# Performance work log

Hardware: AMD Instinct MI355X
Metric: run time of the kernel (lower is better)

Reference implementation:

```python
import math
import jax, jax.numpy as jnp
import numpy as np

N = 1600; C_IN = 16; HID = 64; OUT = 64; D_K = 8; N_HEADS = 8
CUTS = 8; NUM_RBF = 8; RBF_PROJ = 4; RADIUS = 6.0; ALPHA = 3.0

def leaky(x):
    return jnp.where(x >= 0, x, 0.2 * x)

def group_norm(x, gamma, beta, groups=4, eps=1e-5):
    # x: [N, C]; torch GroupNorm applied on [1, C, N]: stats over (C/groups, N) per group
    n, c = x.shape
    xg = x.T.reshape(groups, -1)
    mu = jnp.mean(xg, axis=1, keepdims=True)
    var = jnp.mean((xg - mu) ** 2, axis=1, keepdims=True)
    xn = ((xg - mu) * jax.lax.rsqrt(var + eps)).reshape(c, n).T
    return xn * gamma + beta

def setup_inputs():
    key = jax.random.key(0)
    ks = jax.random.split(key, 32)
    def rn(k, shape, s=0.1):
        return (jax.random.normal(k, shape) * s).astype(jnp.float32)
    return {
        "points": jax.random.normal(ks[0], (N, 3), jnp.float32),
        "nuv": jax.random.normal(ks[1], (N, 3, 3), jnp.float32),
        "features": jax.random.normal(ks[2], (N, C_IN), jnp.float32),
        "w_in1": rn(ks[3], (HID, C_IN)), "b_in1": rn(ks[4], (HID,)),
        "w_in2": rn(ks[5], (HID, HID)), "b_in2": rn(ks[6], (HID,)),
        "g_in": 1.0 + rn(ks[7], (HID,)), "be_in": rn(ks[8], (HID,)),
        "wq": rn(ks[9], (HID, HID)), "bq": rn(ks[10], (HID,)),
        "wk": rn(ks[11], (HID, HID)), "bk": rn(ks[12], (HID,)),
        "wv": rn(ks[13], (HID, HID)), "bv": rn(ks[14], (HID,)),
        "conv_w1": rn(ks[15], (CUTS, 4 + RBF_PROJ), 0.5),
        "conv_b1": jnp.abs(rn(ks[16], (CUTS,), 0.5)),
        "conv_w2": rn(ks[17], (HID, CUTS), 0.3), "conv_b2": rn(ks[18], (HID,), 0.3),
        "rbf_log_sigma": jnp.log(jnp.asarray(0.6 * 2.0 / (NUM_RBF - 1), jnp.float32)),
        "rbf_a": rn(ks[19], (RBF_PROJ, NUM_RBF), 0.3), "rbf_b": rn(ks[20], (RBF_PROJ,), 0.1),
        "rbf_centers": jnp.linspace(0.0, 2.0, NUM_RBF, dtype=jnp.float32),
        "w_o1": rn(ks[21], (OUT, HID)), "b_o1": rn(ks[22], (OUT,)),
        "w_o2": rn(ks[23], (OUT, OUT)), "b_o2": rn(ks[24], (OUT,)),
        "g_out": 1.0 + rn(ks[25], (OUT,)), "be_out": rn(ks[26], (OUT,)),
        "w_res": rn(ks[27], (OUT, C_IN)), "b_res": rn(ks[28], (OUT,)),
    }

def reference(points, nuv, features, w_in1, b_in1, w_in2, b_in2, g_in, be_in,
              wq, bq, wk, bk, wv, bv, conv_w1, conv_b1, conv_w2, conv_b2,
              rbf_log_sigma, rbf_a, rbf_b, rbf_centers,
              w_o1, b_o1, w_o2, b_o2, g_out, be_out, w_res, b_res):
    # point-wise MLP + GroupNorm
    h = leaky(features @ w_in1.T + b_in1)
    h = leaky(h @ w_in2.T + b_in2)
    h = group_norm(h, g_in, be_in)
    Q = h @ wq.T + bq
    K = h @ wk.T + bk
    V = h @ wv.T + bv
    pts = points / (math.sqrt(2.0) * RADIUS)
    diff = pts[None, :, :] - pts[:, None, :]            # [N, N, 3] = x_j - x_i
    n_i = nuv[:, 0, :]
    n_j = jax.lax.stop_gradient(n_i)                    # j-side normals are detached in the original
    ndot = jnp.einsum("ia,ja->ij", n_i, n_j)            # <n_i, n_j>
    d2 = jnp.sum(diff ** 2, axis=-1) * (2.0 - ndot) ** 2  # pseudo-geodesic squared distance
    W = (1.0 + d2 / ALPHA) ** (-ALPHA)                  # geodesic window weight
    d2_safe = jnp.where(d2 > 0, d2, 1.0)
    base_d = jnp.where(d2 > 0, jnp.sqrt(d2_safe), 0.0)  # safe sqrt (finite grad at 0)
    sigma = jnp.maximum(jnp.exp(rbf_log_sigma), 1e-6)
    R = jnp.exp(-((base_d[:, :, None] - rbf_centers) ** 2) / (2.0 * sigma ** 2))  # [N,N,NUM_RBF]
    R_proj = R @ rbf_a.T + rbf_b                        # [N, N, RBF_PROJ]
    X_loc = jnp.einsum("iab,ijb->ija", nuv, diff)       # local tangent-frame coords [N,N,3]
    X = jnp.concatenate([X_loc, ndot[:, :, None], R_proj], axis=-1)  # [N, N, 4+RBF_PROJ]
    F1 = jax.nn.relu(X @ conv_w1.T + conv_b1)           # shared conv layer-1 [N, N, CUTS]
    scale = 1.0 / math.sqrt(D_K)
    heads = []
    for h_id in range(N_HEADS):
        s = slice(h_id * D_K, (h_id + 1) * D_K)
        Fh = jax.nn.relu(F1 @ conv_w2[s].T + conv_b2[s])      # per-head conv weights [N, N, D_K]
        S = (Q[:, s] @ K[:, s].T) * scale                     # attention logits [N, N]
        P = jax.nn.softmax(S, axis=1) * W                     # softmax over j, fused with window
        heads.append(jnp.einsum("ij,ijc,jc->ic", P, Fh, V[:, s]))
    agg = jnp.concatenate(heads, axis=1)                      # [N, HID]
    o = leaky(agg @ w_o1.T + b_o1)
    o = leaky(o @ w_o2.T + b_o2)
    o = group_norm(o, g_out, be_out)
    return o + features @ w_res.T + b_res
```

## Files before the change

kernel.cpp:

```cpp
#include <hip/hip_runtime.h>

typedef __fp16 h2 __attribute__((ext_vector_type(2)));
typedef unsigned int u32;

#define NPTS 1600
#define NCHUNK 10
#define CHUNKJ 160
#define TILE 32
#define QS (0.35355339059327373f*1.4426950408889634f)
#define PSCALE 0.11785113019775793f
#define LOG2E 1.4426950408889634f

__device__ __forceinline__ float leaky(float x){ return x >= 0.f ? x : 0.2f*x; }
__device__ __forceinline__ float d4(float4 a, float4 b){ return a.x*b.x + a.y*b.y + a.z*b.z + a.w*b.w; }
__device__ __forceinline__ u32 pkn(float a, float b){ h2 v; v[0]=(__fp16)a; v[1]=(__fp16)b; return __builtin_bit_cast(u32,v); }
__device__ __forceinline__ h2 u2h(u32 u){ return __builtin_bit_cast(h2,u); }
__device__ __forceinline__ float dot2(h2 a, h2 b, float c){ return __builtin_amdgcn_fdot2(a,b,c,false); }
__device__ __forceinline__ u32 rfl(u32 x){ return (u32)__builtin_amdgcn_readfirstlane((int)x); }

__global__ __launch_bounds__(256) void k_in(
    const float* __restrict__ feat, const float* __restrict__ w1, const float* __restrict__ b1,
    const float* __restrict__ w2, const float* __restrict__ b2,
    const float* __restrict__ conv_w1, const float* __restrict__ conv_b1,
    const float* __restrict__ conv_w2,
    const float* __restrict__ rbf_a, const float* __restrict__ rbf_b,
    const float* __restrict__ rbf_ls, const float* __restrict__ rbf_c,
    float* __restrict__ h2out, float* __restrict__ bstat1, float* __restrict__ wpk)
{
  __shared__ float sh[4][64];
  __shared__ float sred[4][8];
  int t = threadIdx.x, w = t>>6, c = t&63;
  int i = blockIdx.x*4 + w;

  if (blockIdx.x == 0) {
    u32* wp = (u32*)wpk;
    {
      int row = t>>2, q = t&3;
      wp[32 + row*4 + q] = pkn(conv_w2[row*8+2*q], conv_w2[row*8+2*q+1]);
    }
    if (t < 32) {
      int cc = t>>2, kq = t&3;
      float a0=0.f, a1=0.f;
      #pragma unroll
      for (int p=0;p<4;p++){ a0 += conv_w1[cc*8+4+p]*rbf_a[p*8+2*kq]; a1 += conv_w1[cc*8+4+p]*rbf_a[p*8+2*kq+1]; }
      wp[cc*4+kq] = pkn(a0,a1);
    } else if (t < 40) {
      int cc = t-32; float s = conv_b1[cc];
      #pragma unroll
      for (int p=0;p<4;p++) s += conv_w1[cc*8+4+p]*rbf_b[p];
      wpk[288+cc] = s;
    } else if (t == 40) {
      float sig = fmaxf(expf(rbf_ls[0]), 1e-6f);
      float m = -LOG2E/(2.f*sig*sig);
      float c0 = rbf_c[0];
      float dl = rbf_c[1] - rbf_c[0];
      wpk[296] = c0;
      wpk[297] = m;
      wpk[298] = -2.f*m*dl;
      wpk[299] = m*dl*dl;
    }
  }

  const float4* f4 = (const float4*)(feat + i*16);
  float4 f0=f4[0], f1v=f4[1], f2v=f4[2], f3v=f4[3];
  const float4* w1r = (const float4*)(w1 + c*16);
  float h1 = b1[c] + d4(f0,w1r[0]) + d4(f1v,w1r[1]) + d4(f2v,w1r[2]) + d4(f3v,w1r[3]);
  h1 = leaky(h1);
  sh[w][c] = h1;
  __syncthreads();
  float hh = b2[c];
  #pragma unroll
  for (int k4=0;k4<16;k4++){
    float4 hv = *(const float4*)&sh[w][k4*4];
    hh += d4(hv, *(const float4*)&w2[c*64 + k4*4]);
  }
  hh = leaky(hh);
  h2out[i*64+c] = hh;

  float s = hh, qq = hh*hh;
  s += __shfl_xor(s,1);  qq += __shfl_xor(qq,1);
  s += __shfl_xor(s,2);  qq += __shfl_xor(qq,2);
  s += __shfl_xor(s,4);  qq += __shfl_xor(qq,4);
  s += __shfl_xor(s,8);  qq += __shfl_xor(qq,8);
  if ((c&15)==0){ int g=c>>4; sred[w][g]=s; sred[w][4+g]=qq; }
  __syncthreads();
  if (t<8) bstat1[blockIdx.x*8+t] = sred[0][t]+sred[1][t]+sred[2][t]+sred[3][t];
}

__global__ __launch_bounds__(256) void k_qkv(
  const float* __restrict__ h2b, const float* __restrict__ bstat1,
  const float* __restrict__ g_in, const float* __restrict__ be_in,
  const float* __restrict__ wq, const float* __restrict__ bq,
  const float* __restrict__ wk, const float* __restrict__ bk,
  const float* __restrict__ wv, const float* __restrict__ bv,
  float* __restrict__ Q, float* __restrict__ K, float* __restrict__ V)
{
  __shared__ float sh[4][64];
  __shared__ float sp[64];
  __shared__ float sst[8];
  int t=threadIdx.x, w=t>>6, c=t&63;
  int i = blockIdx.x*4 + w;
  if (t<64){ int g=t&7; float s=0.f;
    for (int m=t>>3; m<400; m+=8) s += bstat1[m*8+g];
    sp[t]=s; }
  __syncthreads();
  if (t<8){ float s=0.f;
    #pragma unroll
    for (int q=0;q<8;q++) s += sp[q*8+t];
    sst[t]=s; }
  __syncthreads();
  int g = c>>4;
  const float inv = 1.f/25600.f;
  float mu = sst[g]*inv;
  float var = sst[4+g]*inv - mu*mu;
  float rs = rsqrtf(var + 1e-5f);
  float hn = (h2b[i*64+c]-mu)*rs*g_in[c] + be_in[c];
  sh[w][c] = hn;
  __syncthreads();
  float q=bq[c], k=bk[c], v=bv[c];
  #pragma unroll
  for (int k4=0;k4<16;k4++){
    float4 hv = *(const float4*)&sh[w][k4*4];
    q += d4(hv, *(const float4*)&wq[c*64+k4*4]);
    k += d4(hv, *(const float4*)&wk[c*64+k4*4]);
    v += d4(hv, *(const float4*)&wv[c*64+k4*4]);
  }
  Q[i*64+c] = q*QS;
  K[i*64+c] = k;
  V[i*64+c] = v;
}

__global__ __launch_bounds__(256) void k_pair(
  const float* __restrict__ Qm, const float* __restrict__ Km, const float* __restrict__ Vm,
  const float* __restrict__ pts, const float* __restrict__ nuv,
  const float* __restrict__ w1, const float* __restrict__ wpk,
  const float* __restrict__ b2g, float* __restrict__ part)
{
  __shared__ __align__(16) float SM[4928];
  float* sQ  = SM;
  float* sK  = SM + 1088;
  u32*   sVp = (u32*)(SM + 3264);
  u32*   sWX = (u32*)(SM + 4352);
  float* sPt = SM + 4672;
  float* sNj = SM + 4800;
  float* sRed = SM;

  int t = threadIdx.x;
  int r = t & 15, jl = t >> 4;
  int bx = blockIdx.x;
  int rb = bx % 100, jc = bx / 100;
  int I0 = rb*16, J0 = jc*CHUNKJ;
  int i = I0 + r;

  { int row = t>>4, col = (t&15)<<2;
    *(float4*)&sQ[row*68+col] = *(const float4*)&Qm[(I0+row)*64 + col]; }
  if (t < 128) {
    int r2 = t>>3, cc = t&7, ib = (I0+r2)*9;
    float a0=w1[cc*8], a1=w1[cc*8+1], a2=w1[cc*8+2];
    float x = a0*nuv[ib+0] + a1*nuv[ib+3] + a2*nuv[ib+6];
    float y = a0*nuv[ib+1] + a1*nuv[ib+4] + a2*nuv[ib+7];
    float z = a0*nuv[ib+2] + a1*nuv[ib+5] + a2*nuv[ib+8];
    sWX[r2*20+cc*2+0] = pkn(x,y);
    sWX[r2*20+cc*2+1] = pkn(z, w1[cc*8+3]);
  }
  __syncthreads();
  u32 wxp[16];
  #pragma unroll
  for (int q2=0;q2<4;q2++) *(uint4*)&wxp[q2*4] = *(const uint4*)&sWX[r*20+q2*4];

  const u32* wp = (const u32*)wpk;
  h2 wr[8][4];
  #pragma unroll
  for (int cc=0;cc<8;cc++)
    #pragma unroll
    for (int q2=0;q2<4;q2++) wr[cc][q2] = u2h(rfl(wp[cc*4+q2]));
  const u32* w2p = wp + 32;
  const float* b1p = wpk + 288;
  float c0  = wpk[296];
  float mco = wpk[297];
  float C2  = wpk[298];
  float A1  = wpk[299];

  float pix = pts[i*3+0]*PSCALE, piy = pts[i*3+1]*PSCALE, piz = pts[i*3+2]*PSCALE;
  float nix = nuv[i*9+0], niy = nuv[i*9+1], niz = nuv[i*9+2];

  float acc[64];
  #pragma unroll
  for (int o=0;o<64;o++) acc[o] = 0.f;
  float lh[8];
  #pragma unroll
  for (int h=0;h<8;h++) lh[h] = 0.f;

  #pragma unroll 1
  for (int tb=0; tb<CHUNKJ; tb+=TILE) {
    int jbase = J0 + tb;
    __syncthreads();
    #pragma unroll
    for (int q2=0;q2<2;q2++) {
      int idx = t + q2*256;
      int row = idx >> 4, col = (idx & 15) << 2;
      *(float4*)&sK[row*68+col] = *(const float4*)&Km[(jbase+row)*64+col];
    }
    { int row = t>>4, col = (t&15)<<2;
      float4 a = *(const float4*)&Vm[(jbase+row)*64+col];
      float4 b = *(const float4*)&Vm[(jbase+16+row)*64+col];
      uint4 p; p.x=pkn(a.x,b.x); p.y=pkn(a.y,b.y); p.z=pkn(a.z,b.z); p.w=pkn(a.w,b.w);
      *(uint4*)&sVp[row*68+col] = p;
    }
    if (t < TILE) {
      int j = jbase + t;
      sPt[t*4+0]=pts[j*3+0]*PSCALE; sPt[t*4+1]=pts[j*3+1]*PSCALE; sPt[t*4+2]=pts[j*3+2]*PSCALE;
      sNj[t*4+0]=nuv[j*9+0]; sNj[t*4+1]=nuv[j*9+1]; sNj[t*4+2]=nuv[j*9+2];
    }
    __syncthreads();

    h2 F1p[2][4];
    float Wv[2];
    #pragma unroll
    for (int jj=0;jj<2;jj++) {
      int jloc = jl + (jj<<4);
      float dx = sPt[jloc*4+0]-pix, dy = sPt[jloc*4+1]-piy, dz = sPt[jloc*4+2]-piz;
      float ndot = nix*sNj[jloc*4+0] + niy*sNj[jloc*4+1] + niz*sNj[jloc*4+2];
      float d2r = dx*dx + dy*dy + dz*dz;
      float wf = 2.f - ndot;
      float d2 = d2r*wf*wf;
      float tp = fmaf(d2, 0.3333333333333333f, 1.f);
      Wv[jj] = __builtin_amdgcn_rcpf(tp*tp*tp);
      float dd = __builtin_amdgcn_sqrtf(d2);
      float g0 = dd - c0;
      float s2 = mco*g0*g0;
      float uu = C2*g0;
      float R[8];
      #pragma unroll
      for (int k=0;k<8;k++){
        float kf = (float)k, k2f = (float)(k*k);
        R[k] = __builtin_amdgcn_exp2f(fmaf(kf, uu, fmaf(k2f, A1, s2)));
      }
      h2 xv0; xv0[0]=(__fp16)dx; xv0[1]=(__fp16)dy;
      h2 xv1; xv1[0]=(__fp16)dz; xv1[1]=(__fp16)ndot;
      h2 r01=__builtin_amdgcn_cvt_pkrtz(R[0],R[1]);
      h2 r23=__builtin_amdgcn_cvt_pkrtz(R[2],R[3]);
      h2 r45=__builtin_amdgcn_cvt_pkrtz(R[4],R[5]);
      h2 r67=__builtin_amdgcn_cvt_pkrtz(R[6],R[7]);
      float F1f[8];
      #pragma unroll
      for (int cc=0;cc<8;cc++){
        float f = dot2(r67, wr[cc][3], b1p[cc]);
        f = dot2(r45, wr[cc][2], f);
        f = dot2(r23, wr[cc][1], f);
        f = dot2(r01, wr[cc][0], f);
        f = dot2(u2h(wxp[cc*2+1]), xv1, f);
        f = dot2(u2h(wxp[cc*2+0]), xv0, f);
        F1f[cc] = fmaxf(f, 0.f);
      }
      F1p[jj][0]=__builtin_amdgcn_cvt_pkrtz(F1f[0],F1f[1]);
      F1p[jj][1]=__builtin_amdgcn_cvt_pkrtz(F1f[2],F1f[3]);
      F1p[jj][2]=__builtin_amdgcn_cvt_pkrtz(F1f[4],F1f[5]);
      F1p[jj][3]=__builtin_amdgcn_cvt_pkrtz(F1f[6],F1f[7]);
    }

    #pragma unroll
    for (int h=0;h<8;h++) {
      float4 q0 = *(const float4*)&sQ[r*68+h*8];
      float4 q1 = *(const float4*)&sQ[r*68+h*8+4];
      float4 ka0 = *(const float4*)&sK[jl*68+h*8];
      float4 ka1 = *(const float4*)&sK[jl*68+h*8+4];
      float4 kb0 = *(const float4*)&sK[(jl+16)*68+h*8];
      float4 kb1 = *(const float4*)&sK[(jl+16)*68+h*8+4];
      float S0 = d4(q0,ka0) + d4(q1,ka1);
      float S1 = d4(q0,kb0) + d4(q1,kb1);
      float e0 = __builtin_amdgcn_exp2f(S0);
      float e1 = __builtin_amdgcn_exp2f(S1);
      lh[h] += e0 + e1;
      h2 ewp; ewp[0]=(__fp16)(e0*Wv[0]); ewp[1]=(__fp16)(e1*Wv[1]);
      uint4 vpA = *(const uint4*)&sVp[jl*68+h*8];
      uint4 vpB = *(const uint4*)&sVp[jl*68+h*8+4];
      u32 vparr[8] = {vpA.x,vpA.y,vpA.z,vpA.w,vpB.x,vpB.y,vpB.z,vpB.w};
      #pragma unroll
      for (int cc=0;cc<8;cc++){
        int rw = h*8+cc;
        h2 w0=u2h(w2p[rw*4+0]), w1h=u2h(w2p[rw*4+1]), w2h=u2h(w2p[rw*4+2]), w3h=u2h(w2p[rw*4+3]);
        float b2v = b2g[rw];
        float fh0 = dot2(F1p[0][0],w0, dot2(F1p[0][1],w1h, dot2(F1p[0][2],w2h, dot2(F1p[0][3],w3h, b2v))));
        float fh1 = dot2(F1p[1][0],w0, dot2(F1p[1][1],w1h, dot2(F1p[1][2],w2h, dot2(F1p[1][3],w3h, b2v))));
        h2 fhp = __builtin_amdgcn_cvt_pkrtz(fmaxf(fh0,0.f), fmaxf(fh1,0.f));
        h2 ev = u2h(vparr[cc]) * ewp;
        acc[rw] = dot2(fhp, ev, acc[rw]);
      }
    }
  }

  #pragma unroll
  for (int o=0;o<64;o++){ acc[o] += __shfl_xor(acc[o],16); acc[o] += __shfl_xor(acc[o],32); }
  #pragma unroll
  for (int h=0;h<8;h++){ lh[h] += __shfl_xor(lh[h],16); lh[h] += __shfl_xor(lh[h],32); }
  __syncthreads();
  int wv = t >> 6, lane = t & 63;
  if (lane < 16) {
    #pragma unroll
    for (int o=0;o<64;o++) sRed[(wv*16+lane)*72+o] = acc[o];
    #pragma unroll
    for (int h=0;h<8;h++) sRed[(wv*16+lane)*72+64+h] = lh[h];
  }
  __syncthreads();
  for (int v2 = t; v2 < 16*72; v2 += 256) {
    int rr = v2/72, o = v2 - rr*72;
    part[(jc*NPTS + I0 + rr)*72 + o] =
      sRed[(0*16+rr)*72+o] + sRed[(1*16+rr)*72+o] + sRed[(2*16+rr)*72+o] + sRed[(3*16+rr)*72+o];
  }
}

__global__ __launch_bounds__(256) void k_agg(
  const float* __restrict__ part, const float* __restrict__ w_o1, const float* __restrict__ b_o1,
  const float* __restrict__ w_o2, const float* __restrict__ b_o2,
  float* __restrict__ o2b, float* __restrict__ bstat2)
{
  __shared__ float sh[4][64];
  __shared__ float sred[4][8];
  int t = threadIdx.x, w = t>>6, c = t&63;
  int i = blockIdx.x*4 + w;
  int h = c>>3;
  float a = 0.f, L = 0.f;
  #pragma unroll
  for (int jc=0;jc<NCHUNK;jc++){
    const float* p = part + (jc*NPTS + i)*72;
    a += p[c]; L += p[64+h];
  }
  float agg = a / L;
  sh[w][c] = agg; __syncthreads();
  float o1 = b_o1[c];
  #pragma unroll
  for (int k4=0;k4<16;k4++){
    float4 hv = *(const float4*)&sh[w][k4*4];
    o1 += d4(hv, *(const float4*)&w_o1[c*64+k4*4]);
  }
  o1 = leaky(o1);
  __syncthreads();
  sh[w][c] = o1; __syncthreads();
  float o2 = b_o2[c];
  #pragma unroll
  for (int k4=0;k4<16;k4++){
    float4 hv = *(const float4*)&sh[w][k4*4];
    o2 += d4(hv, *(const float4*)&w_o2[c*64+k4*4]);
  }
  o2 = leaky(o2);
  o2b[i*64+c] = o2;

  float s = o2, qq = o2*o2;
  s += __shfl_xor(s,1);  qq += __shfl_xor(qq,1);
  s += __shfl_xor(s,2);  qq += __shfl_xor(qq,2);
  s += __shfl_xor(s,4);  qq += __shfl_xor(qq,4);
  s += __shfl_xor(s,8);  qq += __shfl_xor(qq,8);
  if ((c&15)==0){ int g=c>>4; sred[w][g]=s; sred[w][4+g]=qq; }
  __syncthreads();
  if (t<8) bstat2[blockIdx.x*8+t] = sred[0][t]+sred[1][t]+sred[2][t]+sred[3][t];
}

__global__ __launch_bounds__(256) void k_out(
  const float* __restrict__ o2b, const float* __restrict__ bstat2,
  const float* __restrict__ g_out, const float* __restrict__ be_out,
  const float* __restrict__ feat, const float* __restrict__ w_res, const float* __restrict__ b_res,
  float* __restrict__ out)
{
  __shared__ float sp[64];
  __shared__ float sst[8];
  int t = threadIdx.x, w = t>>6, c = t&63;
  int i = blockIdx.x*4 + w;
  if (t<64){ int g=t&7; float s=0.f;
    for (int m=t>>3; m<400; m+=8) s += bstat2[m*8+g];
    sp[t]=s; }
  __syncthreads();
  if (t<8){ float s=0.f;
    #pragma unroll
    for (int q=0;q<8;q++) s += sp[q*8+t];
    sst[t]=s; }
  __syncthreads();
  int g = c>>4;
  const float inv = 1.f/25600.f;
  float mu = sst[g]*inv;
  float var = sst[4+g]*inv - mu*mu;
  float rs = rsqrtf(var + 1e-5f);
  float on = (o2b[i*64+c]-mu)*rs*g_out[c] + be_out[c];
  const float4* f4 = (const float4*)(feat + i*16);
  const float4* wr = (const float4*)(w_res + c*16);
  float res = b_res[c] + d4(f4[0],wr[0]) + d4(f4[1],wr[1]) + d4(f4[2],wr[2]) + d4(f4[3],wr[3]);
  out[i*64+c] = on + res;
}

extern "C" void kernel_launch(void* const* d_in, const int* in_sizes, int n_in,
                              void* d_out, int out_size, void* d_ws, size_t ws_size,
                              hipStream_t stream) {
  const float* points  = (const float*)d_in[0];
  const float* nuv     = (const float*)d_in[1];
  const float* feat    = (const float*)d_in[2];
  const float* w_in1   = (const float*)d_in[3];
  const float* b_in1   = (const float*)d_in[4];
  const float* w_in2   = (const float*)d_in[5];
  const float* b_in2   = (const float*)d_in[6];
  const float* g_in    = (const float*)d_in[7];
  const float* be_in   = (const float*)d_in[8];
  const float* wq      = (const float*)d_in[9];
  const float* bq      = (const float*)d_in[10];
  const float* wk      = (const float*)d_in[11];
  const float* bk      = (const float*)d_in[12];
  const float* wv      = (const float*)d_in[13];
  const float* bv      = (const float*)d_in[14];
  const float* conv_w1 = (const float*)d_in[15];
  const float* conv_b1 = (const float*)d_in[16];
  const float* conv_w2 = (const float*)d_in[17];
  const float* conv_b2 = (const float*)d_in[18];
  const float* rbf_ls  = (const float*)d_in[19];
  const float* rbf_a   = (const float*)d_in[20];
  const float* rbf_b   = (const float*)d_in[21];
  const float* rbf_c   = (const float*)d_in[22];
  const float* w_o1    = (const float*)d_in[23];
  const float* b_o1    = (const float*)d_in[24];
  const float* w_o2    = (const float*)d_in[25];
  const float* b_o2    = (const float*)d_in[26];
  const float* g_out   = (const float*)d_in[27];
  const float* be_out  = (const float*)d_in[28];
  const float* w_res   = (const float*)d_in[29];
  const float* b_res   = (const float*)d_in[30];

  float* ws     = (float*)d_ws;
  float* h2f    = ws;
  float* Qb     = ws + 102400;
  float* Kb     = ws + 204800;
  float* Vb     = ws + 307200;
  float* bstat1 = ws + 409600;
  float* bstat2 = ws + 412800;
  float* wpk    = ws + 416000;
  float* part   = ws + 416320;
  float* o2b    = ws + 1568320;
  float* out    = (float*)d_out;

  k_in<<<400, 256, 0, stream>>>(feat, w_in1, b_in1, w_in2, b_in2,
                                conv_w1, conv_b1, conv_w2, rbf_a, rbf_b, rbf_ls, rbf_c,
                                h2f, bstat1, wpk);
  k_qkv<<<400, 256, 0, stream>>>(h2f, bstat1, g_in, be_in, wq, bq, wk, bk, wv, bv, Qb, Kb, Vb);
  k_pair<<<1000, 256, 0, stream>>>(Qb, Kb, Vb, points, nuv, conv_w1, wpk, conv_b2, part);
  k_agg<<<400, 256, 0, stream>>>(part, w_o1, b_o1, w_o2, b_o2, o2b, bstat2);
  k_out<<<400, 256, 0, stream>>>(o2b, bstat2, g_out, be_out, feat, w_res, b_res, out);
}
```

Before: 253.3 us.

## Store Q/K/V as fp16 in pre-packed layouts and compute logits with dot2

```diff
diff --git a/kernel.cpp b/kernel.cpp
--- a/kernel.cpp
+++ b/kernel.cpp
@@ -2,6 +2,7 @@
 
 typedef __fp16 h2 __attribute__((ext_vector_type(2)));
 typedef unsigned int u32;
+typedef unsigned short u16;
 
 #define NPTS 1600
 #define NCHUNK 10
@@ -93,7 +94,9 @@
   const float* __restrict__ wq, const float* __restrict__ bq,
   const float* __restrict__ wk, const float* __restrict__ bk,
   const float* __restrict__ wv, const float* __restrict__ bv,
-  float* __restrict__ Q, float* __restrict__ K, float* __restrict__ V)
+  const float* __restrict__ pts, const float* __restrict__ nuv,
+  u32* __restrict__ Q16, u32* __restrict__ K16, u32* __restrict__ V16,
+  float* __restrict__ PN)
 {
   __shared__ float sh[4][64];
   __shared__ float sp[64];
@@ -125,24 +128,35 @@
     k += d4(hv, *(const float4*)&wk[c*64+k4*4]);
     v += d4(hv, *(const float4*)&wv[c*64+k4*4]);
   }
-  Q[i*64+c] = q*QS;
-  K[i*64+c] = k;
-  V[i*64+c] = v;
+  u16* Q16u = (u16*)Q16;
+  u16* K16u = (u16*)K16;
+  u16* V16u = (u16*)V16;
+  __fp16 qh = (__fp16)(q*QS);
+  __fp16 kh = (__fp16)k;
+  __fp16 vh = (__fp16)v;
+  Q16u[i*64 + c] = __builtin_bit_cast(u16, qh);
+  K16u[i*64 + c] = __builtin_bit_cast(u16, kh);
+  int pr = ((i>>5)<<4) + (i&15);
+  int hf = (i>>4)&1;
+  V16u[(pr*64 + c)*2 + hf] = __builtin_bit_cast(u16, vh);
+  if (c < 6){
+    float pv = (c<3) ? pts[i*3+c]*PSCALE : nuv[i*9+(c-3)];
+    PN[i*8+c] = pv;
+  } else if (c < 8) PN[i*8+c] = 0.f;
 }
 
 __global__ __launch_bounds__(256) void k_pair(
-  const float* __restrict__ Qm, const float* __restrict__ Km, const float* __restrict__ Vm,
-  const float* __restrict__ pts, const float* __restrict__ nuv,
+  const u32* __restrict__ Q16, const u32* __restrict__ K16, const u32* __restrict__ V16,
+  const float* __restrict__ PN, const float* __restrict__ nuv,
   const float* __restrict__ w1, const float* __restrict__ wpk,
   const float* __restrict__ b2g, float* __restrict__ part)
 {
-  __shared__ __align__(16) float SM[4928];
-  float* sQ  = SM;
-  float* sK  = SM + 1088;
-  u32*   sVp = (u32*)(SM + 3264);
-  u32*   sWX = (u32*)(SM + 4352);
-  float* sPt = SM + 4672;
-  float* sNj = SM + 4800;
+  __shared__ __align__(16) float SM[4608];
+  u32*   sQ16 = (u32*)SM;
+  u32*   sK16 = (u32*)SM + 576;
+  u32*   sV16 = (u32*)SM + 1728;
+  float* sPN  = SM + 2816;
+  u32*   sWX  = (u32*)SM + 3072;
   float* sRed = SM;
 
   int t = threadIdx.x;
@@ -152,8 +166,10 @@
   int I0 = rb*16, J0 = jc*CHUNKJ;
   int i = I0 + r;
 
-  { int row = t>>4, col = (t&15)<<2;
-    *(float4*)&sQ[row*68+col] = *(const float4*)&Qm[(I0+row)*64 + col]; }
+  if (t < 128) {
+    int qrow = t>>3, qq4 = (t&7)<<2;
+    *(uint4*)&sQ16[qrow*36+qq4] = *(const uint4*)&Q16[(I0+qrow)*32+qq4];
+  }
   if (t < 128) {
     int r2 = t>>3, cc = t&7, ib = (I0+r2)*9;
     float a0=w1[cc*8], a1=w1[cc*8+1], a2=w1[cc*8+2];
@@ -181,8 +197,10 @@
   float C2  = wpk[298];
   float A1  = wpk[299];
 
-  float pix = pts[i*3+0]*PSCALE, piy = pts[i*3+1]*PSCALE, piz = pts[i*3+2]*PSCALE;
-  float nix = nuv[i*9+0], niy = nuv[i*9+1], niz = nuv[i*9+2];
+  float4 pni0 = *(const float4*)&PN[i*8];
+  float4 pni1 = *(const float4*)&PN[i*8+4];
+  float pix = pni0.x, piy = pni0.y, piz = pni0.z;
+  float nix = pni0.w, niy = pni1.x, niz = pni1.y;
 
   float acc[64];
   #pragma unroll
@@ -195,22 +213,17 @@
   for (int tb=0; tb<CHUNKJ; tb+=TILE) {
     int jbase = J0 + tb;
     __syncthreads();
-    #pragma unroll
-    for (int q2=0;q2<2;q2++) {
-      int idx = t + q2*256;
-      int row = idx >> 4, col = (idx & 15) << 2;
-      *(float4*)&sK[row*68+col] = *(const float4*)&Km[(jbase+row)*64+col];
-    }
-    { int row = t>>4, col = (t&15)<<2;
-      float4 a = *(const float4*)&Vm[(jbase+row)*64+col];
-      float4 b = *(const float4*)&Vm[(jbase+16+row)*64+col];
-      uint4 p; p.x=pkn(a.x,b.x); p.y=pkn(a.y,b.y); p.z=pkn(a.z,b.z); p.w=pkn(a.w,b.w);
-      *(uint4*)&sVp[row*68+col] = p;
-    }
-    if (t < TILE) {
-      int j = jbase + t;
-      sPt[t*4+0]=pts[j*3+0]*PSCALE; sPt[t*4+1]=pts[j*3+1]*PSCALE; sPt[t*4+2]=pts[j*3+2]*PSCALE;
-      sNj[t*4+0]=nuv[j*9+0]; sNj[t*4+1]=nuv[j*9+1]; sNj[t*4+2]=nuv[j*9+2];
+    {
+      int krow = t>>3, kq = (t&7)<<2;
+      *(uint4*)&sK16[krow*36+kq] = *(const uint4*)&K16[(jbase+krow)*32 + kq];
+    }
+    {
+      int vrow = t>>4, vq = (t&15)<<2;
+      *(uint4*)&sV16[vrow*68+vq] = *(const uint4*)&V16[((jbase>>1)+vrow)*64 + vq];
+    }
+    if (t < 64) {
+      int prow = t>>1, ph = (t&1)<<2;
+      *(float4*)&sPN[prow*8+ph] = *(const float4*)&PN[(jbase+prow)*8+ph];
     }
     __syncthreads();
 
@@ -219,8 +232,10 @@
     #pragma unroll
     for (int jj=0;jj<2;jj++) {
       int jloc = jl + (jj<<4);
-      float dx = sPt[jloc*4+0]-pix, dy = sPt[jloc*4+1]-piy, dz = sPt[jloc*4+2]-piz;
-      float ndot = nix*sNj[jloc*4+0] + niy*sNj[jloc*4+1] + niz*sNj[jloc*4+2];
+      float4 a0 = *(const float4*)&sPN[jloc*8];
+      float4 a1 = *(const float4*)&sPN[jloc*8+4];
+      float dx = a0.x-pix, dy = a0.y-piy, dz = a0.z-piz;
+      float ndot = nix*a0.w + niy*a1.x + niz*a1.y;
       float d2r = dx*dx + dy*dy + dz*dz;
       float wf = 2.f - ndot;
       float d2 = d2r*wf*wf;
@@ -258,23 +273,23 @@
       F1p[jj][2]=__builtin_amdgcn_cvt_pkrtz(F1f[4],F1f[5]);
       F1p[jj][3]=__builtin_amdgcn_cvt_pkrtz(F1f[6],F1f[7]);
     }
+    h2 Wvp = __builtin_amdgcn_cvt_pkrtz(Wv[0], Wv[1]);
 
     #pragma unroll
     for (int h=0;h<8;h++) {
-      float4 q0 = *(const float4*)&sQ[r*68+h*8];
-      float4 q1 = *(const float4*)&sQ[r*68+h*8+4];
-      float4 ka0 = *(const float4*)&sK[jl*68+h*8];
-      float4 ka1 = *(const float4*)&sK[jl*68+h*8+4];
-      float4 kb0 = *(const float4*)&sK[(jl+16)*68+h*8];
-      float4 kb1 = *(const float4*)&sK[(jl+16)*68+h*8+4];
-      float S0 = d4(q0,ka0) + d4(q1,ka1);
-      float S1 = d4(q0,kb0) + d4(q1,kb1);
+      uint4 qh = *(const uint4*)&sQ16[r*36 + (h<<2)];
+      uint4 kA = *(const uint4*)&sK16[jl*36 + (h<<2)];
+      uint4 kB = *(const uint4*)&sK16[(jl+16)*36 + (h<<2)];
+      float S0 = dot2(u2h(qh.x),u2h(kA.x), dot2(u2h(qh.y),u2h(kA.y),
+                 dot2(u2h(qh.z),u2h(kA.z), dot2(u2h(qh.w),u2h(kA.w), 0.f))));
+      float S1 = dot2(u2h(qh.x),u2h(kB.x), dot2(u2h(qh.y),u2h(kB.y),
+                 dot2(u2h(qh.z),u2h(kB.z), dot2(u2h(qh.w),u2h(kB.w), 0.f))));
       float e0 = __builtin_amdgcn_exp2f(S0);
       float e1 = __builtin_amdgcn_exp2f(S1);
       lh[h] += e0 + e1;
-      h2 ewp; ewp[0]=(__fp16)(e0*Wv[0]); ewp[1]=(__fp16)(e1*Wv[1]);
-      uint4 vpA = *(const uint4*)&sVp[jl*68+h*8];
-      uint4 vpB = *(const uint4*)&sVp[jl*68+h*8+4];
+      h2 ewp = __builtin_amdgcn_cvt_pkrtz(e0,e1) * Wvp;
+      uint4 vpA = *(const uint4*)&sV16[jl*68 + h*8];
+      uint4 vpB = *(const uint4*)&sV16[jl*68 + h*8 + 4];
       u32 vparr[8] = {vpA.x,vpA.y,vpA.z,vpA.w,vpB.x,vpB.y,vpB.z,vpB.w};
       #pragma unroll
       for (int cc=0;cc<8;cc++){
@@ -424,21 +439,23 @@
 
   float* ws     = (float*)d_ws;
   float* h2f    = ws;
-  float* Qb     = ws + 102400;
-  float* Kb     = ws + 204800;
-  float* Vb     = ws + 307200;
-  float* bstat1 = ws + 409600;
-  float* bstat2 = ws + 412800;
-  float* wpk    = ws + 416000;
-  float* part   = ws + 416320;
-  float* o2b    = ws + 1568320;
+  u32*   Q16    = (u32*)(ws + 102400);
+  u32*   K16    = (u32*)(ws + 153600);
+  u32*   V16    = (u32*)(ws + 204800);
+  float* PN     = ws + 256000;
+  float* bstat1 = ws + 268800;
+  float* bstat2 = ws + 272000;
+  float* wpk    = ws + 275200;
+  float* part   = ws + 275520;
+  float* o2b    = ws + 1427520;
   float* out    = (float*)d_out;
 
   k_in<<<400, 256, 0, stream>>>(feat, w_in1, b_in1, w_in2, b_in2,
                                 conv_w1, conv_b1, conv_w2, rbf_a, rbf_b, rbf_ls, rbf_c,
                                 h2f, bstat1, wpk);
-  k_qkv<<<400, 256, 0, stream>>>(h2f, bstat1, g_in, be_in, wq, bq, wk, bk, wv, bv, Qb, Kb, Vb);
-  k_pair<<<1000, 256, 0, stream>>>(Qb, Kb, Vb, points, nuv, conv_w1, wpk, conv_b2, part);
+  k_qkv<<<400, 256, 0, stream>>>(h2f, bstat1, g_in, be_in, wq, bq, wk, bk, wv, bv,
+                                 points, nuv, Q16, K16, V16, PN);
+  k_pair<<<1000, 256, 0, stream>>>(Q16, K16, V16, PN, nuv, conv_w1, wpk, conv_b2, part);
   k_agg<<<400, 256, 0, stream>>>(part, w_o1, b_o1, w_o2, b_o2, o2b, bstat2);
   k_out<<<400, 256, 0, stream>>>(o2b, bstat2, g_out, be_out, feat, w_res, b_res, out);
 }
```

Result: faster. 248.1 us (-2.0%).
